# Kernel tuning notes

Measured on AMD Instinct MI355X. Metric: run time of the kernel, lower is better.

The kernel has to match this reference:

```python
import jax, jax.numpy as jnp
import numpy as np

KERNEL = 11
BERT_DIM = 768
B, S, T = 2, 16, 64
EPS = 1e-6  # cosine-similarity eps (matches nn.CosineSimilarity(eps=1e-06))
CLAMP_MIN = 1e-6


def _kernel_mus(n):
    mus = [1.0]
    if n == 1:
        return mus
    b = 2.0 / (n - 1)
    mus.append(1.0 - b / 2.0)
    for i in range(1, n - 1):
        mus.append(mus[i] - b)
    return mus

MU = jnp.asarray(_kernel_mus(KERNEL), dtype=jnp.float32)      # (K,)
SIGMA = jnp.asarray([0.001] + [0.1] * (KERNEL - 1), dtype=jnp.float32)  # (K,)


def setup_inputs() -> dict:
    key = jax.random.key(0)
    ks = jax.random.split(key, 8)
    s = 0.02
    return {
        "claim_reps": jax.random.normal(ks[0], (B, T, BERT_DIM), jnp.float32),
        "sentence_token_reps": jax.random.normal(ks[1], (B, S, T, BERT_DIM), jnp.float32),
        "claim_token_mask": jnp.ones((B, T), dtype=bool),
        "token_mask": jnp.ones((B, S, T), dtype=bool),
        "w_sel": jax.random.normal(ks[2], (KERNEL, 1), jnp.float32) * s,
        "b_sel": jnp.zeros((1,), jnp.float32),
        "w_g1": jax.random.normal(ks[3], (2 * BERT_DIM, 128), jnp.float32) * s,
        "b_g1": jnp.zeros((128,), jnp.float32),
        "w_g2": jax.random.normal(ks[4], (128, 1), jnp.float32) * s,
        "b_g2": jnp.zeros((1,), jnp.float32),
        "w_rat": jax.random.normal(ks[5], (KERNEL, 1), jnp.float32) * s,
        "b_rat": jnp.zeros((1,), jnp.float32),
        "w_lab": jax.random.normal(ks[6], (2 * BERT_DIM, 3), jnp.float32) * s,
        "b_lab": jnp.zeros((3,), jnp.float32),
    }


def _forward(claim_reps, reps, token_mask,
             w_sel, b_sel, w_g1, b_g1, w_g2, b_g2, w_rat, b_rat, w_lab, b_lab):
    maskf = token_mask.astype(jnp.float32)           # (B,S,T)
    b_, s_, t_, d_ = reps.shape

    # ---------------- edge kernel ----------------
    # sim[b,i,j,p,q] = cos(reps[b,i,p], reps[b,j,q])
    norms = jnp.linalg.norm(reps, axis=-1)           # (B,S,T)
    dot = jnp.einsum('bipd,bjqd->bijpq', reps, reps)  # (B,S1,S2,T1,T2)
    sim = dot / jnp.maximum(norms[:, :, None, :, None] * norms[:, None, :, None, :], EPS)
    rbf = jnp.exp(-0.5 * ((sim[..., None] - MU) / SIGMA) ** 2)   # (B,S1,S2,T1,T2,K)
    # original mask broadcasts mask[b,s2,t1] over the summed T2 axis
    pool = rbf.sum(axis=4) * maskf[:, None, :, :, None]           # (B,S1,S2,T1,K)
    Ke = jnp.log(jnp.clip(pool, CLAMP_MIN, None))
    logits = Ke @ w_sel + b_sel                                   # (B,S1,S2,T1,1)
    m2 = jnp.broadcast_to(token_mask[:, None, :, :, None], logits.shape)
    attn = jax.nn.softmax(jnp.where(m2, logits, -10000.0), axis=3)  # softmax over T1
    # reps_exp[b,i,j,t,:] = reps[b,j,t,:]
    z_hat = jnp.einsum('bjtd,bijt->bijd', reps, attn[..., 0])     # (B,S1,S2,D)
    z = reps[:, :, 0, :]                                          # (B,S,D) CLS tokens
    z_exp = jnp.broadcast_to(z[:, None, :, :], z_hat.shape)       # z[b,s2]
    h = jax.nn.relu(jnp.concatenate([z_exp, z_hat], axis=-1) @ w_g1 + b_g1)
    beta = jax.nn.softmax(h @ w_g2 + b_g2, axis=1)                # softmax over S1
    v = jnp.concatenate([jnp.sum(beta * z_hat, axis=1), z], axis=-1)  # (B,S,2D)
    sentence_label_pred = jax.nn.softmax(v @ w_lab + b_lab, axis=-1)  # (B,S,3)

    # ---------------- node kernel ----------------
    # NOTE: the original broadcasts BOTH operands over t2, so sim depends only on
    # (b,s,t1): cos(claim[b,t1], reps[b,s,t1]); the T2 sum multiplies by n_token.
    nc = jnp.linalg.norm(claim_reps, axis=-1)                     # (B,T)
    dotn = jnp.einsum('btd,bstd->bst', claim_reps, reps)          # (B,S,T)
    simn = dotn / jnp.maximum(nc[:, None, :] * norms, EPS)
    rbfn = jnp.exp(-0.5 * ((simn[..., None] - MU) / SIGMA) ** 2)  # (B,S,T,K)
    pooln = rbfn * maskf[..., None] * jnp.float32(t_)
    phi = jnp.mean(jnp.log(jnp.clip(pooln, CLAMP_MIN, None)), axis=-2)  # (B,S,K)
    rationale = jax.nn.softmax(phi @ w_rat + b_rat, axis=1)       # (B,S,1)

    return jnp.sum(sentence_label_pred * rationale, axis=1)       # (B,3)


def reference(claim_reps, sentence_token_reps, claim_token_mask, token_mask,
              w_sel, b_sel, w_g1, b_g1, w_g2, b_g2, w_rat, b_rat, w_lab, b_lab):
    # claim_token_mask is accepted by the original forward but never used
    return _forward(claim_reps, sentence_token_reps, token_mask,
                    w_sel, b_sel, w_g1, b_g1, w_g2, b_g2,
                    w_rat, b_rat, w_lab, b_lab)
```

## Files before the change

kernel.cpp:

```cpp
#include <hip/hip_runtime.h>
#include <hip/hip_bf16.h>

#define NK 11

typedef __bf16 bf16_t;
typedef __bf16 bf16x4 __attribute__((ext_vector_type(4)));
typedef __bf16 bf16x8 __attribute__((ext_vector_type(8)));
typedef float f32x4 __attribute__((ext_vector_type(4)));

__device__ __constant__ float MU_C[NK]   = {1.0f,0.9f,0.7f,0.5f,0.3f,0.1f,-0.1f,-0.3f,-0.5f,-0.7f,-0.9f};
__device__ __constant__ float ISIG_C[NK] = {1000.0f,10.0f,10.0f,10.0f,10.0f,10.0f,10.0f,10.0f,10.0f,10.0f,10.0f};

#define E_P16 8886110.5f
#define E_P12 162754.796875f
#define E_P4  54.598150033f
#define E_M8  3.35462628e-4f
#define E_M12 6.14421235e-6f

__global__ __launch_bounds__(256) void kp_prep(
    const float* __restrict__ reps, const float* __restrict__ w_g1,
    const float* __restrict__ b_rat,
    bf16_t* __restrict__ repsb, float* __restrict__ norms,
    bf16_t* __restrict__ w1t, float* __restrict__ phir, float* __restrict__ out)
{
    __shared__ bf16_t wt[128*137];
    const int tid = threadIdx.x;
    const int bid = blockIdx.x;
    if (bid < 256) {
        const int tok = bid * 8 + (tid >> 5);
        const int ln  = tid & 31;
        const float* src = reps + (size_t)tok * 768 + ln * 24;
        bf16_t*      dst = repsb + (size_t)tok * 768 + ln * 24;
        float s = 0.f;
        #pragma unroll
        for (int x = 0; x < 24; x += 4) {
            f32x4 f = *(const f32x4*)(src + x);
            bf16x4 h = {(bf16_t)f[0], (bf16_t)f[1], (bf16_t)f[2], (bf16_t)f[3]};
            *(bf16x4*)(dst + x) = h;
            s += f[0]*f[0] + f[1]*f[1] + f[2]*f[2] + f[3]*f[3];
        }
        #pragma unroll
        for (int off = 16; off; off >>= 1) s += __shfl_xor(s, off, 32);
        if (ln == 0) norms[tok] = sqrtf(s);
        if (bid == 0) {
            if (tid < 6) out[tid] = 0.f;
            if (tid >= 32 && tid < 64) phir[tid - 32] = b_rat[0];
        }
    } else {
        const int td = bid - 256;
        const float* wsrc = w_g1 + (size_t)td * 128 * 128;
        #pragma unroll
        for (int rep = 0; rep < 16; ++rep) {
            int linear = rep*256 + tid;
            int row = linear >> 5, c4 = (linear & 31) * 4;
            f32x4 v = *(const f32x4*)(wsrc + (size_t)row*128 + c4);
            wt[(c4+0)*137 + row] = (bf16_t)v[0];
            wt[(c4+1)*137 + row] = (bf16_t)v[1];
            wt[(c4+2)*137 + row] = (bf16_t)v[2];
            wt[(c4+3)*137 + row] = (bf16_t)v[3];
        }
        __syncthreads();
        #pragma unroll
        for (int rep = 0; rep < 8; ++rep) {
            int linear = rep*256 + tid;
            int c = linear >> 4, d8 = (linear & 15) * 8;
            bf16x8 h8;
            #pragma unroll
            for (int e = 0; e < 8; ++e) h8[e] = wt[c*137 + d8 + e];
            *(bf16x8*)&w1t[(size_t)c*1536 + td*128 + d8] = h8;
        }
    }
}

__global__ __launch_bounds__(512, 4) void ka_simpool(
    const float* __restrict__ claim,
    const bf16_t* __restrict__ repsb, const float* __restrict__ norms,
    const float* __restrict__ w_sel, const float* __restrict__ b_sel,
    const float* __restrict__ w_rat,
    bf16_t* __restrict__ zhatb, float* __restrict__ phir)
{
    __shared__ __align__(16) bf16_t As[64*264];
    __shared__ __align__(16) bf16_t Bs[64*264];
    __shared__ float normI[64], normJ[64], attnS[64];
    __shared__ float phiLoc;

    const int tid = threadIdx.x;
    const int bid = blockIdx.x;

    if (bid >= 512) {
        const int pid = bid - 512;
        const int b = pid >> 5, rem = pid & 31, s_ = rem >> 1, tg = rem & 1;
        if (tid == 0) phiLoc = 0.f;
        __syncthreads();
        const int tok = tg*32 + (tid >> 4), part = tid & 15;
        const float*  cp = claim + (size_t)(b*64 + tok)*768 + part*48;
        const bf16_t* rp = repsb + (size_t)((b*16 + s_)*64 + tok)*768 + part*48;
        float sd = 0.f, sc = 0.f;
        #pragma unroll
        for (int x = 0; x < 48; x += 8) {
            f32x4 c0 = *(const f32x4*)(cp + x);
            f32x4 c1 = *(const f32x4*)(cp + x + 4);
            bf16x8 r8 = *(const bf16x8*)(rp + x);
            sd += c0[0]*(float)r8[0] + c0[1]*(float)r8[1] + c0[2]*(float)r8[2] + c0[3]*(float)r8[3]
                + c1[0]*(float)r8[4] + c1[1]*(float)r8[5] + c1[2]*(float)r8[6] + c1[3]*(float)r8[7];
            sc += c0[0]*c0[0]+c0[1]*c0[1]+c0[2]*c0[2]+c0[3]*c0[3]
                + c1[0]*c1[0]+c1[1]*c1[1]+c1[2]*c1[2]+c1[3]*c1[3];
        }
        #pragma unroll
        for (int off = 8; off; off >>= 1) {
            sd += __shfl_xor(sd, off, 16);
            sc += __shfl_xor(sc, off, 16);
        }
        if (part == 0) {
            float nr = norms[(b*16 + s_)*64 + tok];
            float simn = sd / fmaxf(sqrtf(sc)*nr, 1e-6f);
            float contrib = 0.f;
            #pragma unroll
            for (int k = 0; k < NK; ++k) {
                float dd = (simn - MU_C[k]) * ISIG_C[k];
                float pool = __expf(-0.5f*dd*dd) * 64.0f;
                contrib += w_rat[k] * __logf(fmaxf(pool, 1e-6f));
            }
            atomicAdd(&phiLoc, contrib * (1.0f/64.0f));
        }
        __syncthreads();
        if (tid == 0) atomicAdd(&phir[b*16 + s_], phiLoc);
        return;
    }

    const int b = bid >> 8, rem = bid & 255, i = rem >> 4, j = rem & 15;
    const bf16_t* Rib = repsb + (size_t)((b*16 + i)*64) * 768;
    const bf16_t* Rjb = repsb + (size_t)((b*16 + j)*64) * 768;

    if (tid < 64)       normI[tid]    = norms[(b*16 + i)*64 + tid];
    else if (tid < 128) normJ[tid-64] = norms[(b*16 + j)*64 + (tid-64)];

    const int wave = tid >> 6, lane = tid & 63;
    const int wr = wave & 1, wc = wave >> 1;
    const int m16 = lane & 15, q4 = lane >> 4;

    f32x4 acc0 = {0.f,0.f,0.f,0.f}, acc1 = {0.f,0.f,0.f,0.f};
    {
        const int srow = tid >> 5, sc8 = (tid & 31) * 8;
        bf16x8 ga[4], gb[4];
        #pragma unroll
        for (int r = 0; r < 4; ++r) {
            ga[r] = *(const bf16x8*)(Rib + (size_t)(srow + 16*r)*768 + sc8);
            gb[r] = *(const bf16x8*)(Rjb + (size_t)(srow + 16*r)*768 + sc8);
        }
        for (int ko = 0; ko < 3; ++ko) {
            __syncthreads();
            #pragma unroll
            for (int r = 0; r < 4; ++r) {
                *(bf16x8*)&As[(srow + 16*r)*264 + sc8] = ga[r];
                *(bf16x8*)&Bs[(srow + 16*r)*264 + sc8] = gb[r];
            }
            __syncthreads();
            if (ko < 2) {
                #pragma unroll
                for (int r = 0; r < 4; ++r) {
                    ga[r] = *(const bf16x8*)(Rib + (size_t)(srow + 16*r)*768 + (ko+1)*256 + sc8);
                    gb[r] = *(const bf16x8*)(Rjb + (size_t)(srow + 16*r)*768 + (ko+1)*256 + sc8);
                }
            }
            #pragma unroll
            for (int ks = 0; ks < 8; ++ks) {
                int kb = ks*32 + q4*8;
                bf16x8 a0 = *(const bf16x8*)&As[(32*wr      + m16)*264 + kb];
                bf16x8 a1 = *(const bf16x8*)&As[(32*wr + 16 + m16)*264 + kb];
                bf16x8 b0 = *(const bf16x8*)&Bs[(16*wc      + m16)*264 + kb];
                acc0 = __builtin_amdgcn_mfma_f32_16x16x32_bf16(a0, b0, acc0, 0, 0, 0);
                acc1 = __builtin_amdgcn_mfma_f32_16x16x32_bf16(a1, b0, acc1, 0, 0, 0);
            }
        }
    }
    __syncthreads();

    float* simb = (float*)As;
    {
        int q = wc*16 + m16;
        float nj = normJ[q];
        #pragma unroll
        for (int tr = 0; tr < 2; ++tr) {
            f32x4 a = tr ? acc1 : acc0;
            #pragma unroll
            for (int e = 0; e < 4; ++e) {
                int p = 32*wr + 16*tr + q4*4 + e;
                float v = a[e] / fmaxf(normI[p]*nj, 1e-6f);
                if (i == j && p == q) v = 1.0f;
                simb[p*65 + q] = v;
            }
        }
    }
    __syncthreads();

    float* poolp = (float*)Bs;
    {
        int p = tid & 63, qg = tid >> 6;
        float pk[NK];
        #pragma unroll
        for (int k = 0; k < NK; ++k) pk[k] = 0.f;
        #pragma unroll
        for (int qi = 0; qi < 8; ++qi) {
            float s = simb[p*65 + qg*8 + qi];
            float d0 = (s - 1.0f) * 1000.f;
            pk[0] += __expf(-0.5f*d0*d0);
            float R  = __expf(-20.f*s);
            float d1 = s - 0.9f;
            float E  = __expf(-50.f*d1*d1);
            pk[1] += E;
            E *= R * E_P16; pk[2] += E;
            E *= R * E_P12; pk[3] += E;
            float d4 = s - 0.3f;
            E = __expf(-50.f*d4*d4);
            pk[4] += E;
            E *= R * E_P4;  pk[5] += E;
            E *= R;         pk[6] += E;
            float d7 = s + 0.3f;
            E = __expf(-50.f*d7*d7);
            pk[7] += E;
            E *= R * E_M8;  pk[8] += E;
            E *= R * E_M12; pk[9] += E;
            float d10 = s + 0.9f;
            pk[10] += __expf(-50.f*d10*d10);
        }
        #pragma unroll
        for (int k = 0; k < NK; ++k) poolp[p*89 + qg*11 + k] = pk[k];
    }
    __syncthreads();

    if (tid < 64) {
        float lg = b_sel[0];
        #pragma unroll
        for (int k = 0; k < NK; ++k) {
            float pool = 0.f;
            #pragma unroll
            for (int qg = 0; qg < 8; ++qg) pool += poolp[tid*89 + qg*11 + k];
            lg += __logf(fmaxf(pool, 1e-6f)) * w_sel[k];
        }
        float m = lg;
        #pragma unroll
        for (int off = 32; off; off >>= 1) m = fmaxf(m, __shfl_xor(m, off));
        float e = __expf(lg - m), ssum = e;
        #pragma unroll
        for (int off = 32; off; off >>= 1) ssum += __shfl_xor(ssum, off);
        attnS[tid] = e / ssum;
    }
    __syncthreads();

    {
        const int th = tid >> 7, dg = tid & 127;
        float a8[8] = {0.f,0.f,0.f,0.f,0.f,0.f,0.f,0.f};
        if (dg < 96) {
            const bf16_t* src = Rjb + (size_t)(th*16)*768 + dg*8;
            #pragma unroll 4
            for (int t = 0; t < 16; ++t) {
                bf16x8 r = *(const bf16x8*)(src + (size_t)t*768);
                float at = attnS[th*16 + t];
                #pragma unroll
                for (int e = 0; e < 8; ++e) a8[e] += at * (float)r[e];
            }
        }
        float* zp = (float*)As;
        if (th > 0 && dg < 96) {
            #pragma unroll
            for (int e = 0; e < 8; ++e) zp[(th-1)*768 + dg*8 + e] = a8[e];
        }
        __syncthreads();
        if (th == 0 && dg < 96) {
            bf16x8 o;
            #pragma unroll
            for (int e = 0; e < 8; ++e)
                o[e] = (bf16_t)(a8[e] + zp[dg*8+e] + zp[768 + dg*8+e] + zp[1536 + dg*8+e]);
            *(bf16x8*)&zhatb[(size_t)bid*768 + dg*8] = o;
        }
    }
}

__global__ __launch_bounds__(256) void kc_final(
    const float* __restrict__ reps, const bf16_t* __restrict__ zhatb,
    const bf16_t* __restrict__ w1t,
    const float* __restrict__ b_g1, const float* __restrict__ w_g2,
    const float* __restrict__ b_g2, const float* __restrict__ phir,
    const float* __restrict__ w_lab, const float* __restrict__ b_lab,
    float* __restrict__ out)
{
    __shared__ __align__(16) bf16_t Ws[128*136];
    __shared__ __align__(16) bf16_t As[16*136];
    __shared__ float gpart[4][16];
    __shared__ float betaS[16], zl[768], vs[768], Lm[3];
    __shared__ float ratS;

    const int tid = threadIdx.x;
    const int b = blockIdx.x >> 4, j = blockIdx.x & 15;
    const int wave = tid >> 6, lane = tid & 63;
    const int m16 = lane & 15, q4 = lane >> 4;

    for (int d = tid; d < 768; d += 256) zl[d] = reps[(size_t)((b*16 + j)*64)*768 + d];

    f32x4 acc0 = {0.f,0.f,0.f,0.f}, acc1 = {0.f,0.f,0.f,0.f};
    for (int ck = 0; ck < 12; ++ck) {
        __syncthreads();
        #pragma unroll
        for (int rep = 0; rep < 8; ++rep) {
            int linear = rep*256 + tid;
            int c = linear >> 4, k8 = (linear & 15)*8;
            *(bf16x8*)&Ws[c*136 + k8] = *(const bf16x8*)&w1t[(size_t)c*1536 + ck*128 + k8];
        }
        if (ck < 6) {
            #pragma unroll
            for (int rep = 0; rep < 2; ++rep) {
                int linear = rep*256 + tid;
                int ii = linear >> 5, c4 = (linear & 31)*4;
                f32x4 v = *(const f32x4*)(reps + (size_t)((b*16 + ii)*64)*768 + ck*128 + c4);
                bf16x4 h = {(bf16_t)v[0],(bf16_t)v[1],(bf16_t)v[2],(bf16_t)v[3]};
                *(bf16x4*)&As[ii*136 + c4] = h;
            }
        } else {
            int ii = tid >> 4, k8 = (tid & 15)*8;
            *(bf16x8*)&As[ii*136 + k8] =
                *(const bf16x8*)&zhatb[(size_t)((b*16 + ii)*16 + j)*768 + (ck-6)*128 + k8];
        }
        __syncthreads();
        #pragma unroll
        for (int ks = 0; ks < 4; ++ks) {
            bf16x8 a  = *(const bf16x8*)&As[m16*136 + ks*32 + q4*8];
            bf16x8 b0 = *(const bf16x8*)&Ws[(wave*32 + m16)*136 + ks*32 + q4*8];
            bf16x8 b1 = *(const bf16x8*)&Ws[(wave*32 + 16 + m16)*136 + ks*32 + q4*8];
            acc0 = __builtin_amdgcn_mfma_f32_16x16x32_bf16(a, b0, acc0, 0, 0, 0);
            acc1 = __builtin_amdgcn_mfma_f32_16x16x32_bf16(a, b1, acc1, 0, 0, 0);
        }
    }
    {
        int c0 = wave*32 + m16, c1 = wave*32 + 16 + m16;
        float bg0 = b_g1[c0], bg1 = b_g1[c1];
        float wg0 = w_g2[c0], wg1 = w_g2[c1];
        float ge[4];
        #pragma unroll
        for (int e = 0; e < 4; ++e)
            ge[e] = fmaxf(acc0[e] + bg0, 0.f)*wg0 + fmaxf(acc1[e] + bg1, 0.f)*wg1;
        #pragma unroll
        for (int off = 1; off < 16; off <<= 1) {
            #pragma unroll
            for (int e = 0; e < 4; ++e) ge[e] += __shfl_xor(ge[e], off);
        }
        if (m16 == 0) {
            #pragma unroll
            for (int e = 0; e < 4; ++e) gpart[wave][q4*4 + e] = ge[e];
        }
    }
    __syncthreads();
    if (tid < 16) {
        float x = gpart[0][tid] + gpart[1][tid] + gpart[2][tid] + gpart[3][tid] + b_g2[0];
        float m = x;
        #pragma unroll
        for (int off = 8; off; off >>= 1) m = fmaxf(m, __shfl_xor(m, off, 16));
        float e = __expf(x - m), ss = e;
        #pragma unroll
        for (int off = 8; off; off >>= 1) ss += __shfl_xor(ss, off, 16);
        betaS[tid] = e / ss;
    }
    __syncthreads();
    {
        float va[8] = {0.f,0.f,0.f,0.f,0.f,0.f,0.f,0.f};
        const int ih = (tid >= 96 && tid < 192) ? 1 : 0;
        const int dg = tid - ih*96;
        if (tid < 192) {
            const bf16_t* src = zhatb + (size_t)((b*16 + ih*8)*16 + j)*768 + dg*8;
            #pragma unroll
            for (int ii = 0; ii < 8; ++ii) {
                bf16x8 r = *(const bf16x8*)(src + (size_t)ii*16*768);
                float bt = betaS[ih*8 + ii];
                #pragma unroll
                for (int e = 0; e < 8; ++e) va[e] += bt * (float)r[e];
            }
        }
        __syncthreads();
        float* vsp = (float*)Ws;
        if (ih == 1) {
            #pragma unroll
            for (int e = 0; e < 8; ++e) vsp[dg*8 + e] = va[e];
        }
        __syncthreads();
        if (tid < 96) {
            #pragma unroll
            for (int e = 0; e < 8; ++e) vs[tid*8 + e] = va[e] + vsp[tid*8 + e];
        }
    }
    __syncthreads();
    if (tid < 192) {
        int m = tid >> 6, ln = tid & 63;
        float s = 0.f;
        #pragma unroll 4
        for (int d = ln; d < 768; d += 64)
            s += vs[d]*w_lab[(size_t)d*3 + m] + zl[d]*w_lab[(size_t)(768 + d)*3 + m];
        #pragma unroll
        for (int off = 32; off; off >>= 1) s += __shfl_xor(s, off);
        if (ln == 0) Lm[m] = s + b_lab[m];
    }
    if (tid >= 192 && tid < 208) {
        int s_ = tid - 192;
        float x = phir[b*16 + s_], m = x;
        #pragma unroll
        for (int off = 8; off; off >>= 1) m = fmaxf(m, __shfl_xor(m, off, 16));
        float e = __expf(x - m), ss = e;
        #pragma unroll
        for (int off = 8; off; off >>= 1) ss += __shfl_xor(ss, off, 16);
        if (s_ == j) ratS = e / ss;
    }
    __syncthreads();
    if (tid == 0) {
        float m = fmaxf(Lm[0], fmaxf(Lm[1], Lm[2]));
        float e0 = __expf(Lm[0]-m), e1 = __expf(Lm[1]-m), e2 = __expf(Lm[2]-m);
        float inv = 1.f / (e0+e1+e2);
        float r = ratS;
        atomicAdd(&out[b*3+0], r*e0*inv);
        atomicAdd(&out[b*3+1], r*e1*inv);
        atomicAdd(&out[b*3+2], r*e2*inv);
    }
}

extern "C" void kernel_launch(void* const* d_in, const int* in_sizes, int n_in,
                              void* d_out, int out_size, void* d_ws, size_t ws_size,
                              hipStream_t stream) {
    const float* claim = (const float*)d_in[0];
    const float* reps  = (const float*)d_in[1];
    const float* w_sel = (const float*)d_in[4];
    const float* b_sel = (const float*)d_in[5];
    const float* w_g1  = (const float*)d_in[6];
    const float* b_g1  = (const float*)d_in[7];
    const float* w_g2  = (const float*)d_in[8];
    const float* b_g2  = (const float*)d_in[9];
    const float* w_rat = (const float*)d_in[10];
    const float* b_rat = (const float*)d_in[11];
    const float* w_lab = (const float*)d_in[12];
    const float* b_lab = (const float*)d_in[13];

    float*  ws    = (float*)d_ws;
    bf16_t* repsb = (bf16_t*)ws;
    float*  norms = ws + 786432;
    bf16_t* zhatb = (bf16_t*)(ws + 786432 + 2048);
    bf16_t* w1t   = (bf16_t*)(ws + 786432 + 2048 + 196608);
    float*  phir  = ws + 786432 + 2048 + 196608 + 98304;
    float*  out   = (float*)d_out;

    hipLaunchKernelGGL(kp_prep,    dim3(268), dim3(256), 0, stream,
                       reps, w_g1, b_rat, repsb, norms, w1t, phir, out);
    hipLaunchKernelGGL(ka_simpool, dim3(576), dim3(512), 0, stream,
                       claim, repsb, norms, w_sel, b_sel, w_rat, zhatb, phir);
    hipLaunchKernelGGL(kc_final,   dim3(32),  dim3(256), 0, stream,
                       reps, zhatb, w1t, b_g1, w_g2, b_g2, phir, w_lab, b_lab, out);
}
```

Measured before the change: 126.6 us.

## Fold claim-sentence RBF into simpool blocks and widen final kernel to 512 threads

```diff
diff --git a/kernel.cpp b/kernel.cpp
--- a/kernel.cpp
+++ b/kernel.cpp
@@ -17,20 +17,47 @@
 #define E_M8  3.35462628e-4f
 #define E_M12 6.14421235e-6f
 
+__device__ __forceinline__ float rbf_logit_contrib(float s, const float* w) {
+    float contrib = 0.f;
+    float d0 = (s - 1.0f) * 1000.f;
+    contrib += w[0] * __logf(fmaxf(__expf(-0.5f*d0*d0) * 64.f, 1e-6f));
+    float R  = __expf(-20.f*s);
+    float d1 = s - 0.9f;
+    float E  = __expf(-50.f*d1*d1);
+    contrib += w[1] * __logf(fmaxf(E * 64.f, 1e-6f));
+    E *= R * E_P16; contrib += w[2] * __logf(fmaxf(E * 64.f, 1e-6f));
+    E *= R * E_P12; contrib += w[3] * __logf(fmaxf(E * 64.f, 1e-6f));
+    float d4 = s - 0.3f;
+    E = __expf(-50.f*d4*d4);
+    contrib += w[4] * __logf(fmaxf(E * 64.f, 1e-6f));
+    E *= R * E_P4;  contrib += w[5] * __logf(fmaxf(E * 64.f, 1e-6f));
+    E *= R;         contrib += w[6] * __logf(fmaxf(E * 64.f, 1e-6f));
+    float d7 = s + 0.3f;
+    E = __expf(-50.f*d7*d7);
+    contrib += w[7] * __logf(fmaxf(E * 64.f, 1e-6f));
+    E *= R * E_M8;  contrib += w[8] * __logf(fmaxf(E * 64.f, 1e-6f));
+    E *= R * E_M12; contrib += w[9] * __logf(fmaxf(E * 64.f, 1e-6f));
+    float d10 = s + 0.9f;
+    contrib += w[10] * __logf(fmaxf(__expf(-50.f*d10*d10) * 64.f, 1e-6f));
+    return contrib;
+}
+
 __global__ __launch_bounds__(256) void kp_prep(
-    const float* __restrict__ reps, const float* __restrict__ w_g1,
-    const float* __restrict__ b_rat,
+    const float* __restrict__ reps, const float* __restrict__ claim,
+    const float* __restrict__ w_g1, const float* __restrict__ b_rat,
     bf16_t* __restrict__ repsb, float* __restrict__ norms,
+    bf16_t* __restrict__ claimb, float* __restrict__ nc,
     bf16_t* __restrict__ w1t, float* __restrict__ phir, float* __restrict__ out)
 {
     __shared__ bf16_t wt[128*137];
     const int tid = threadIdx.x;
     const int bid = blockIdx.x;
-    if (bid < 256) {
-        const int tok = bid * 8 + (tid >> 5);
+    if (bid < 272) {
+        const bool isClaim = (bid >= 256);
+        const int tok = (isClaim ? (bid - 256) : bid) * 8 + (tid >> 5);
         const int ln  = tid & 31;
-        const float* src = reps + (size_t)tok * 768 + ln * 24;
-        bf16_t*      dst = repsb + (size_t)tok * 768 + ln * 24;
+        const float* src = (isClaim ? claim : reps) + (size_t)tok * 768 + ln * 24;
+        bf16_t*      dst = (isClaim ? claimb : repsb) + (size_t)tok * 768 + ln * 24;
         float s = 0.f;
         #pragma unroll
         for (int x = 0; x < 24; x += 4) {
@@ -41,13 +68,15 @@
         }
         #pragma unroll
         for (int off = 16; off; off >>= 1) s += __shfl_xor(s, off, 32);
-        if (ln == 0) norms[tok] = sqrtf(s);
+        if (ln == 0) {
+            if (isClaim) nc[tok] = sqrtf(s); else norms[tok] = sqrtf(s);
+        }
         if (bid == 0) {
             if (tid < 6) out[tid] = 0.f;
             if (tid >= 32 && tid < 64) phir[tid - 32] = b_rat[0];
         }
     } else {
-        const int td = bid - 256;
+        const int td = bid - 272;
         const float* wsrc = w_g1 + (size_t)td * 128 * 128;
         #pragma unroll
         for (int rep = 0; rep < 16; ++rep) {
@@ -73,8 +102,8 @@
 }
 
 __global__ __launch_bounds__(512, 4) void ka_simpool(
-    const float* __restrict__ claim,
     const bf16_t* __restrict__ repsb, const float* __restrict__ norms,
+    const bf16_t* __restrict__ claimb, const float* __restrict__ nc,
     const float* __restrict__ w_sel, const float* __restrict__ b_sel,
     const float* __restrict__ w_rat,
     bf16_t* __restrict__ zhatb, float* __restrict__ phir)
@@ -82,52 +111,9 @@
     __shared__ __align__(16) bf16_t As[64*264];
     __shared__ __align__(16) bf16_t Bs[64*264];
     __shared__ float normI[64], normJ[64], attnS[64];
-    __shared__ float phiLoc;
 
     const int tid = threadIdx.x;
     const int bid = blockIdx.x;
-
-    if (bid >= 512) {
-        const int pid = bid - 512;
-        const int b = pid >> 5, rem = pid & 31, s_ = rem >> 1, tg = rem & 1;
-        if (tid == 0) phiLoc = 0.f;
-        __syncthreads();
-        const int tok = tg*32 + (tid >> 4), part = tid & 15;
-        const float*  cp = claim + (size_t)(b*64 + tok)*768 + part*48;
-        const bf16_t* rp = repsb + (size_t)((b*16 + s_)*64 + tok)*768 + part*48;
-        float sd = 0.f, sc = 0.f;
-        #pragma unroll
-        for (int x = 0; x < 48; x += 8) {
-            f32x4 c0 = *(const f32x4*)(cp + x);
-            f32x4 c1 = *(const f32x4*)(cp + x + 4);
-            bf16x8 r8 = *(const bf16x8*)(rp + x);
-            sd += c0[0]*(float)r8[0] + c0[1]*(float)r8[1] + c0[2]*(float)r8[2] + c0[3]*(float)r8[3]
-                + c1[0]*(float)r8[4] + c1[1]*(float)r8[5] + c1[2]*(float)r8[6] + c1[3]*(float)r8[7];
-            sc += c0[0]*c0[0]+c0[1]*c0[1]+c0[2]*c0[2]+c0[3]*c0[3]
-                + c1[0]*c1[0]+c1[1]*c1[1]+c1[2]*c1[2]+c1[3]*c1[3];
-        }
-        #pragma unroll
-        for (int off = 8; off; off >>= 1) {
-            sd += __shfl_xor(sd, off, 16);
-            sc += __shfl_xor(sc, off, 16);
-        }
-        if (part == 0) {
-            float nr = norms[(b*16 + s_)*64 + tok];
-            float simn = sd / fmaxf(sqrtf(sc)*nr, 1e-6f);
-            float contrib = 0.f;
-            #pragma unroll
-            for (int k = 0; k < NK; ++k) {
-                float dd = (simn - MU_C[k]) * ISIG_C[k];
-                float pool = __expf(-0.5f*dd*dd) * 64.0f;
-                contrib += w_rat[k] * __logf(fmaxf(pool, 1e-6f));
-            }
-            atomicAdd(&phiLoc, contrib * (1.0f/64.0f));
-        }
-        __syncthreads();
-        if (tid == 0) atomicAdd(&phir[b*16 + s_], phiLoc);
-        return;
-    }
-
     const int b = bid >> 8, rem = bid & 255, i = rem >> 4, j = rem & 15;
     const bf16_t* Rib = repsb + (size_t)((b*16 + i)*64) * 768;
     const bf16_t* Rjb = repsb + (size_t)((b*16 + j)*64) * 768;
@@ -136,6 +122,34 @@
     else if (tid < 128) normJ[tid-64] = norms[(b*16 + j)*64 + (tid-64)];
 
     const int wave = tid >> 6, lane = tid & 63;
+
+    if (wave < 4) {
+        const int u = bid*4 + wave;
+        const int pb = u >> 10, prem = u & 1023, s_ = prem >> 6, ptok = prem & 63;
+        const bf16_t* cp = claimb + (size_t)(pb*64 + ptok)*768 + lane*12;
+        const bf16_t* rp = repsb + (size_t)((pb*16 + s_)*64 + ptok)*768 + lane*12;
+        bf16x8 c8 = *(const bf16x8*)cp;
+        bf16x4 c4 = *(const bf16x4*)(cp + 8);
+        bf16x8 r8 = *(const bf16x8*)rp;
+        bf16x4 r4 = *(const bf16x4*)(rp + 8);
+        float sd = 0.f;
+        #pragma unroll
+        for (int e = 0; e < 8; ++e) sd += (float)c8[e] * (float)r8[e];
+        #pragma unroll
+        for (int e = 0; e < 4; ++e) sd += (float)c4[e] * (float)r4[e];
+        #pragma unroll
+        for (int off = 32; off; off >>= 1) sd += __shfl_xor(sd, off);
+        if (lane == 0) {
+            float ncl = nc[pb*64 + ptok];
+            float nr  = norms[(pb*16 + s_)*64 + ptok];
+            float simn = sd / fmaxf(ncl*nr, 1e-6f);
+            float w[NK];
+            #pragma unroll
+            for (int k = 0; k < NK; ++k) w[k] = w_rat[k];
+            atomicAdd(&phir[pb*16 + s_], rbf_logit_contrib(simn, w) * (1.0f/64.0f));
+        }
+    }
+
     const int wr = wave & 1, wc = wave >> 1;
     const int m16 = lane & 15, q4 = lane >> 4;
 
@@ -277,7 +291,7 @@
     }
 }
 
-__global__ __launch_bounds__(256) void kc_final(
+__global__ __launch_bounds__(512) void kc_final(
     const float* __restrict__ reps, const bf16_t* __restrict__ zhatb,
     const bf16_t* __restrict__ w1t,
     const float* __restrict__ b_g1, const float* __restrict__ w_g2,
@@ -287,7 +301,7 @@
 {
     __shared__ __align__(16) bf16_t Ws[128*136];
     __shared__ __align__(16) bf16_t As[16*136];
-    __shared__ float gpart[4][16];
+    __shared__ float gpart[8][16];
     __shared__ float betaS[16], zl[768], vs[768], Lm[3];
     __shared__ float ratS;
 
@@ -296,49 +310,45 @@
     const int wave = tid >> 6, lane = tid & 63;
     const int m16 = lane & 15, q4 = lane >> 4;
 
-    for (int d = tid; d < 768; d += 256) zl[d] = reps[(size_t)((b*16 + j)*64)*768 + d];
-
-    f32x4 acc0 = {0.f,0.f,0.f,0.f}, acc1 = {0.f,0.f,0.f,0.f};
+    for (int d = tid; d < 768; d += 512) zl[d] = reps[(size_t)((b*16 + j)*64)*768 + d];
+
+    f32x4 acc = {0.f,0.f,0.f,0.f};
     for (int ck = 0; ck < 12; ++ck) {
         __syncthreads();
         #pragma unroll
-        for (int rep = 0; rep < 8; ++rep) {
-            int linear = rep*256 + tid;
+        for (int rep = 0; rep < 4; ++rep) {
+            int linear = rep*512 + tid;
             int c = linear >> 4, k8 = (linear & 15)*8;
             *(bf16x8*)&Ws[c*136 + k8] = *(const bf16x8*)&w1t[(size_t)c*1536 + ck*128 + k8];
         }
         if (ck < 6) {
-            #pragma unroll
-            for (int rep = 0; rep < 2; ++rep) {
-                int linear = rep*256 + tid;
-                int ii = linear >> 5, c4 = (linear & 31)*4;
+            {
+                int ii = tid >> 5, c4 = (tid & 31)*4;
                 f32x4 v = *(const f32x4*)(reps + (size_t)((b*16 + ii)*64)*768 + ck*128 + c4);
                 bf16x4 h = {(bf16_t)v[0],(bf16_t)v[1],(bf16_t)v[2],(bf16_t)v[3]};
                 *(bf16x4*)&As[ii*136 + c4] = h;
             }
         } else {
-            int ii = tid >> 4, k8 = (tid & 15)*8;
-            *(bf16x8*)&As[ii*136 + k8] =
-                *(const bf16x8*)&zhatb[(size_t)((b*16 + ii)*16 + j)*768 + (ck-6)*128 + k8];
+            if (tid < 256) {
+                int ii = tid >> 4, k8 = (tid & 15)*8;
+                *(bf16x8*)&As[ii*136 + k8] =
+                    *(const bf16x8*)&zhatb[(size_t)((b*16 + ii)*16 + j)*768 + (ck-6)*128 + k8];
+            }
         }
         __syncthreads();
         #pragma unroll
         for (int ks = 0; ks < 4; ++ks) {
             bf16x8 a  = *(const bf16x8*)&As[m16*136 + ks*32 + q4*8];
-            bf16x8 b0 = *(const bf16x8*)&Ws[(wave*32 + m16)*136 + ks*32 + q4*8];
-            bf16x8 b1 = *(const bf16x8*)&Ws[(wave*32 + 16 + m16)*136 + ks*32 + q4*8];
-            acc0 = __builtin_amdgcn_mfma_f32_16x16x32_bf16(a, b0, acc0, 0, 0, 0);
-            acc1 = __builtin_amdgcn_mfma_f32_16x16x32_bf16(a, b1, acc1, 0, 0, 0);
-        }
-    }
-    {
-        int c0 = wave*32 + m16, c1 = wave*32 + 16 + m16;
-        float bg0 = b_g1[c0], bg1 = b_g1[c1];
-        float wg0 = w_g2[c0], wg1 = w_g2[c1];
+            bf16x8 b0 = *(const bf16x8*)&Ws[(wave*16 + m16)*136 + ks*32 + q4*8];
+            acc = __builtin_amdgcn_mfma_f32_16x16x32_bf16(a, b0, acc, 0, 0, 0);
+        }
+    }
+    {
+        int c0 = wave*16 + m16;
+        float bg0 = b_g1[c0], wg0 = w_g2[c0];
         float ge[4];
         #pragma unroll
-        for (int e = 0; e < 4; ++e)
-            ge[e] = fmaxf(acc0[e] + bg0, 0.f)*wg0 + fmaxf(acc1[e] + bg1, 0.f)*wg1;
+        for (int e = 0; e < 4; ++e) ge[e] = fmaxf(acc[e] + bg0, 0.f)*wg0;
         #pragma unroll
         for (int off = 1; off < 16; off <<= 1) {
             #pragma unroll
@@ -351,7 +361,9 @@
     }
     __syncthreads();
     if (tid < 16) {
-        float x = gpart[0][tid] + gpart[1][tid] + gpart[2][tid] + gpart[3][tid] + b_g2[0];
+        float x = b_g2[0];
+        #pragma unroll
+        for (int w = 0; w < 8; ++w) x += gpart[w][tid];
         float m = x;
         #pragma unroll
         for (int off = 8; off; off >>= 1) m = fmaxf(m, __shfl_xor(m, off, 16));
@@ -363,28 +375,28 @@
     __syncthreads();
     {
         float va[8] = {0.f,0.f,0.f,0.f,0.f,0.f,0.f,0.f};
-        const int ih = (tid >= 96 && tid < 192) ? 1 : 0;
-        const int dg = tid - ih*96;
-        if (tid < 192) {
-            const bf16_t* src = zhatb + (size_t)((b*16 + ih*8)*16 + j)*768 + dg*8;
-            #pragma unroll
-            for (int ii = 0; ii < 8; ++ii) {
+        const int th = tid >> 7, dg = tid & 127;
+        if (dg < 96) {
+            const bf16_t* src = zhatb + (size_t)((b*16 + th*4)*16 + j)*768 + dg*8;
+            #pragma unroll
+            for (int ii = 0; ii < 4; ++ii) {
                 bf16x8 r = *(const bf16x8*)(src + (size_t)ii*16*768);
-                float bt = betaS[ih*8 + ii];
+                float bt = betaS[th*4 + ii];
                 #pragma unroll
                 for (int e = 0; e < 8; ++e) va[e] += bt * (float)r[e];
             }
         }
         __syncthreads();
         float* vsp = (float*)Ws;
-        if (ih == 1) {
-            #pragma unroll
-            for (int e = 0; e < 8; ++e) vsp[dg*8 + e] = va[e];
-        }
-        __syncthreads();
-        if (tid < 96) {
-            #pragma unroll
-            for (int e = 0; e < 8; ++e) vs[tid*8 + e] = va[e] + vsp[tid*8 + e];
+        if (th > 0 && dg < 96) {
+            #pragma unroll
+            for (int e = 0; e < 8; ++e) vsp[(th-1)*768 + dg*8 + e] = va[e];
+        }
+        __syncthreads();
+        if (th == 0 && dg < 96) {
+            #pragma unroll
+            for (int e = 0; e < 8; ++e)
+                vs[dg*8 + e] = va[e] + vsp[dg*8+e] + vsp[768 + dg*8+e] + vsp[1536 + dg*8+e];
         }
     }
     __syncthreads();
@@ -436,18 +448,20 @@
     const float* w_lab = (const float*)d_in[12];
     const float* b_lab = (const float*)d_in[13];
 
-    float*  ws    = (float*)d_ws;
-    bf16_t* repsb = (bf16_t*)ws;
-    float*  norms = ws + 786432;
-    bf16_t* zhatb = (bf16_t*)(ws + 786432 + 2048);
-    bf16_t* w1t   = (bf16_t*)(ws + 786432 + 2048 + 196608);
-    float*  phir  = ws + 786432 + 2048 + 196608 + 98304;
-    float*  out   = (float*)d_out;
-
-    hipLaunchKernelGGL(kp_prep,    dim3(268), dim3(256), 0, stream,
-                       reps, w_g1, b_rat, repsb, norms, w1t, phir, out);
-    hipLaunchKernelGGL(ka_simpool, dim3(576), dim3(512), 0, stream,
-                       claim, repsb, norms, w_sel, b_sel, w_rat, zhatb, phir);
-    hipLaunchKernelGGL(kc_final,   dim3(32),  dim3(256), 0, stream,
+    float*  ws     = (float*)d_ws;
+    bf16_t* repsb  = (bf16_t*)ws;
+    float*  norms  = ws + 786432;
+    bf16_t* claimb = (bf16_t*)(ws + 788480);
+    float*  ncv    = ws + 837632;
+    bf16_t* zhatb  = (bf16_t*)(ws + 837760);
+    bf16_t* w1t    = (bf16_t*)(ws + 1034368);
+    float*  phir   = ws + 1132672;
+    float*  out    = (float*)d_out;
+
+    hipLaunchKernelGGL(kp_prep,    dim3(284), dim3(256), 0, stream,
+                       reps, claim, w_g1, b_rat, repsb, norms, claimb, ncv, w1t, phir, out);
+    hipLaunchKernelGGL(ka_simpool, dim3(512), dim3(512), 0, stream,
+                       repsb, norms, claimb, ncv, w_sel, b_sel, w_rat, zhatb, phir);
+    hipLaunchKernelGGL(kc_final,   dim3(32),  dim3(512), 0, stream,
                        reps, zhatb, w1t, b_g1, w_g2, b_g2, phir, w_lab, b_lab, out);
 }
```

Result: slower. 145.5 us (+14.9%).
